# Kernel tuning notes

Hardware: AMD Instinct MI355X
Metric: run time of the kernel (lower is better)

Reference implementation:

```python
import jax, jax.numpy as jnp
import numpy as np

COUNT = 8
OUT_F = 32
IN_F = 1024
QN, QP = -128, 127  # int8 LSQ range used by nnue-pytorch


def _grad_scale(x, s):
    # forward: x ; backward: grad * s
    return x * s + jax.lax.stop_gradient(x - x * s)


def _round_pass(x):
    # forward: round(x) ; backward: identity (STE)
    return x + jax.lax.stop_gradient(jnp.round(x) - x)


def quantized_weight(weight, log_alpha_w):
    # LSQ (learned step size quantization), per-output-row step size
    alpha = jnp.exp(log_alpha_w)[:, None]                    # [O*C, 1]
    g = 1.0 / np.sqrt(float(weight.size) * QP)
    alpha = _grad_scale(alpha, jnp.asarray(g, weight.dtype))
    w_s = jnp.clip(weight / alpha, QN, QP)
    return _round_pass(w_s) * alpha                          # [O*C, I]


def setup_inputs() -> dict:
    key = jax.random.key(0)
    k1, k2, k3, k4, k5 = jax.random.split(key, 5)
    B = 8192
    x = jax.random.normal(k1, (B, IN_F), dtype=jnp.float32)
    ls_indices = jax.random.randint(k2, (B,), 0, COUNT).astype(jnp.int64)
    weight = jax.random.normal(k3, (COUNT * OUT_F, IN_F), dtype=jnp.float32) * 0.02
    bias = jax.random.normal(k4, (COUNT * OUT_F,), dtype=jnp.float32) * 0.01
    log_alpha_w = jax.random.normal(k5, (COUNT * OUT_F,), dtype=jnp.float32) * 0.1 - 5.0
    return {"x": x, "ls_indices": ls_indices, "weight": weight,
            "bias": bias, "log_alpha_w": log_alpha_w}


def reference(x, ls_indices, weight, bias, log_alpha_w):
    wq = quantized_weight(weight, log_alpha_w)               # [C*O, I]
    w_r = wq.reshape(COUNT, OUT_F, IN_F)                     # [C, O, I]
    b_r = bias.reshape(COUNT, OUT_F)                         # [C, O]
    idx = ls_indices.astype(jnp.int32)
    w_sel = w_r[idx]                                         # [B, O, I] gather
    b_sel = b_r[idx]                                         # [B, O]
    out = jnp.einsum("boi,bi->bo", w_sel, x)                # per-sample matvec
    return out + b_sel
```

## Files before the change

kernel.cpp:

```cpp
#include <hip/hip_runtime.h>


#define IN_F   1024
#define OUT_F  32
#define NCLS   8
#define NB     8192
#define KSPLIT 8
#define KCH    (IN_F / KSPLIT)
#define GRIDX  40

typedef __attribute__((ext_vector_type(8))) __bf16 bf16x8;
typedef __attribute__((ext_vector_type(4))) float  f32x4;

__device__ __forceinline__ unsigned short f2bf(float f) {
    unsigned int u = __builtin_bit_cast(unsigned int, f);
    u += 0x7FFFu + ((u >> 16) & 1u);
    return (unsigned short)(u >> 16);
}

__device__ __forceinline__ bf16x8 pack8(float4 v0, float4 v1) {
    union { unsigned short u[8]; bf16x8 v; } r;
    r.u[0] = f2bf(v0.x); r.u[1] = f2bf(v0.y); r.u[2] = f2bf(v0.z); r.u[3] = f2bf(v0.w);
    r.u[4] = f2bf(v1.x); r.u[5] = f2bf(v1.y); r.u[6] = f2bf(v1.z); r.u[7] = f2bf(v1.w);
    return r.v;
}

__global__ __launch_bounds__(256) void prep_kernel(
    const float* __restrict__ weight, const float* __restrict__ law,
    const unsigned int* __restrict__ lsw, const float* __restrict__ bias,
    float* __restrict__ alf, unsigned short* __restrict__ wq,
    int* __restrict__ counts, unsigned short* __restrict__ buckets,
    float* __restrict__ out)
{
    int t = threadIdx.x;
    if (blockIdx.x < NCLS * OUT_F) {
        int row = blockIdx.x;
        float a = expf(law[row]);
        if (t == 0) alf[row] = a;
        float4 v = ((const float4*)(weight + (size_t)row * IN_F))[t];
        ushort4 p;
        p.x = f2bf(rintf(fminf(fmaxf(v.x / a, -128.f), 127.f)));
        p.y = f2bf(rintf(fminf(fmaxf(v.y / a, -128.f), 127.f)));
        p.z = f2bf(rintf(fminf(fmaxf(v.z / a, -128.f), 127.f)));
        p.w = f2bf(rintf(fminf(fmaxf(v.w / a, -128.f), 127.f)));
        ((ushort4*)(wq + (size_t)row * IN_F))[t] = p;
        return;
    }
    int blk = blockIdx.x - NCLS * OUT_F;
    int b = blk * 256 + t;
    __shared__ int lcnt[NCLS];
    __shared__ int lbase[NCLS];
    __shared__ int s_is64;
    if (t < NCLS) lcnt[t] = 0;
    if (t == 0) s_is64 = 1;
    __syncthreads();
    if (t < 128) {
        if (lsw[2 * (blk * 128 + t) + 1] != 0u) atomicAnd(&s_is64, 0);
    }
    __syncthreads();
    int c = s_is64 ? (int)lsw[2 * b] : (int)lsw[b];
    const float4* bb = (const float4*)(bias + c * OUT_F);
    float4* ob = (float4*)(out + (size_t)b * OUT_F);
    #pragma unroll
    for (int i = 0; i < OUT_F / 4; ++i) ob[i] = bb[i];
    int lpos = atomicAdd(&lcnt[c], 1);
    __syncthreads();
    if (t < NCLS) lbase[t] = atomicAdd(&counts[t], lcnt[t]);
    __syncthreads();
    buckets[c * NB + lbase[c] + lpos] = (unsigned short)b;
}

__global__ __launch_bounds__(128) void gemm_kernel(
    const float* __restrict__ x, const float* __restrict__ alf,
    const unsigned short* __restrict__ wq,
    const int* __restrict__ counts, const unsigned short* __restrict__ buckets,
    float* __restrict__ out)
{
    int c  = blockIdx.y;
    int kq = blockIdx.z;
    int cnt = counts[c];
    int t = threadIdx.x;
    int wave = t >> 6, lane = t & 63;
    int fr = lane & 15, fq = lane >> 4;
    int k0 = kq * KCH;

    const unsigned short* wrow0 = wq + (size_t)(c * OUT_F + fr) * IN_F + k0 + fq * 8;
    const unsigned short* wrow1 = wrow0 + 16 * IN_F;
    bf16x8 Bf0[KCH / 32], Bf1[KCH / 32];
    #pragma unroll
    for (int kk = 0; kk < KCH / 32; ++kk) {
        Bf0[kk] = *(const bf16x8*)(wrow0 + kk * 32);
        Bf1[kk] = *(const bf16x8*)(wrow1 + kk * 32);
    }
    float a0 = alf[c * OUT_F + fr];
    float a1 = alf[c * OUT_F + 16 + fr];

    for (int tile = blockIdx.x * 2 + wave; tile * 16 < cnt; tile += GRIDX * 2) {
        int start = tile * 16;
        int nvalid = min(16, cnt - start);
        int j = min(fr, nvalid - 1);
        int srow = (int)buckets[c * NB + start + j];
        const float* xr = x + (size_t)srow * IN_F + k0 + fq * 8;
        f32x4 acc0 = {0.f, 0.f, 0.f, 0.f};
        f32x4 acc1 = {0.f, 0.f, 0.f, 0.f};
        #pragma unroll
        for (int kk = 0; kk < KCH / 32; ++kk) {
            float4 v0 = *(const float4*)(xr + kk * 32);
            float4 v1 = *(const float4*)(xr + kk * 32 + 4);
            bf16x8 a = pack8(v0, v1);
            acc0 = __builtin_amdgcn_mfma_f32_16x16x32_bf16(a, Bf0[kk], acc0, 0, 0, 0);
            acc1 = __builtin_amdgcn_mfma_f32_16x16x32_bf16(a, Bf1[kk], acc1, 0, 0, 0);
        }
        #pragma unroll
        for (int reg = 0; reg < 4; ++reg) {
            int m = fq * 4 + reg;
            int sr = __shfl(srow, m);
            if (m < nvalid) {
                atomicAdd(&out[(size_t)sr * OUT_F + fr],      acc0[reg] * a0);
                atomicAdd(&out[(size_t)sr * OUT_F + 16 + fr], acc1[reg] * a1);
            }
        }
    }
}

extern "C" void kernel_launch(void* const* d_in, const int* in_sizes, int n_in,
                              void* d_out, int out_size, void* d_ws, size_t ws_size,
                              hipStream_t stream)
{
    (void)in_sizes; (void)n_in; (void)out_size; (void)ws_size;
    const float*        x      = (const float*)d_in[0];
    const unsigned int* ls     = (const unsigned int*)d_in[1];
    const float*        weight = (const float*)d_in[2];
    const float*        bias   = (const float*)d_in[3];
    const float*        law    = (const float*)d_in[4];
    float*              out    = (float*)d_out;

    char* ws = (char*)d_ws;
    int*            counts  = (int*)ws;
    float*          alf     = (float*)(ws + 64);
    unsigned short* wq      = (unsigned short*)(ws + 64 + 1024);
    unsigned short* buckets = (unsigned short*)(ws + 64 + 1024 + 524288);

    hipMemsetAsync(counts, 0, NCLS * sizeof(int), stream);
    prep_kernel<<<NCLS * OUT_F + NB / 256, 256, 0, stream>>>(
        weight, law, ls, bias, alf, wq, counts, buckets, out);
    gemm_kernel<<<dim3(GRIDX, NCLS, KSPLIT), 128, 0, stream>>>(
        x, alf, wq, counts, buckets, out);
}
```

Measured before the change: 92.70 us.

## Replace atomic bucketing with single-block scan, drop memset, early-exit idle gemm blocks

The prep kernel now runs as 65 blocks of 1024 threads. 64 blocks quantize weights at four rows per block. One block buckets all 8192 samples using a wave-level shuffle prefix scan over packed 16-bit per-class counters, so it no longer needs global atomics. It writes the class counts directly, which removes the hipMemsetAsync launch. The gemm kernel exits early for blocks that have no tiles. The risk is that one block now serially handles all bucketing and bias initialization for 8192 rows, which could become a tail on the critical path.

```diff
diff --git a/kernel.cpp b/kernel.cpp
--- a/kernel.cpp
+++ b/kernel.cpp
@@ -25,7 +25,7 @@
     return r.v;
 }
 
-__global__ __launch_bounds__(256) void prep_kernel(
+__global__ __launch_bounds__(1024) void prep_kernel(
     const float* __restrict__ weight, const float* __restrict__ law,
     const unsigned int* __restrict__ lsw, const float* __restrict__ bias,
     float* __restrict__ alf, unsigned short* __restrict__ wq,
@@ -33,41 +33,84 @@
     float* __restrict__ out)
 {
     int t = threadIdx.x;
-    if (blockIdx.x < NCLS * OUT_F) {
-        int row = blockIdx.x;
+    if (blockIdx.x < 64) {
+        int row = blockIdx.x * 4 + (t >> 8);
+        int c4  = t & 255;
         float a = expf(law[row]);
-        if (t == 0) alf[row] = a;
-        float4 v = ((const float4*)(weight + (size_t)row * IN_F))[t];
+        if (c4 == 0) alf[row] = a;
+        float4 v = ((const float4*)(weight + (size_t)row * IN_F))[c4];
         ushort4 p;
         p.x = f2bf(rintf(fminf(fmaxf(v.x / a, -128.f), 127.f)));
         p.y = f2bf(rintf(fminf(fmaxf(v.y / a, -128.f), 127.f)));
         p.z = f2bf(rintf(fminf(fmaxf(v.z / a, -128.f), 127.f)));
         p.w = f2bf(rintf(fminf(fmaxf(v.w / a, -128.f), 127.f)));
-        ((ushort4*)(wq + (size_t)row * IN_F))[t] = p;
+        ((ushort4*)(wq + (size_t)row * IN_F))[c4] = p;
         return;
     }
-    int blk = blockIdx.x - NCLS * OUT_F;
-    int b = blk * 256 + t;
-    __shared__ int lcnt[NCLS];
-    __shared__ int lbase[NCLS];
+    int lane = t & 63, wv = t >> 6;
     __shared__ int s_is64;
-    if (t < NCLS) lcnt[t] = 0;
+    __shared__ unsigned int wtot[16][4];
+    __shared__ unsigned int wbase[16][4];
     if (t == 0) s_is64 = 1;
     __syncthreads();
-    if (t < 128) {
-        if (lsw[2 * (blk * 128 + t) + 1] != 0u) atomicAnd(&s_is64, 0);
+    int bad = 0;
+    #pragma unroll
+    for (int j = 0; j < 4; ++j) bad |= (lsw[2 * (j * 1024 + t) + 1] != 0u);
+    if (bad) atomicAnd(&s_is64, 0);
+    __syncthreads();
+    int is64 = s_is64;
+    unsigned int cpack = 0;
+    unsigned int cnt[4] = {0, 0, 0, 0};
+    #pragma unroll
+    for (int j = 0; j < 8; ++j) {
+        int b = j * 1024 + t;
+        int c = is64 ? (int)lsw[2 * b] : (int)lsw[b];
+        cpack |= (unsigned int)c << (j * 4);
+        cnt[c >> 1] += 1u << ((c & 1) * 16);
+    }
+    unsigned int inc[4] = {cnt[0], cnt[1], cnt[2], cnt[3]};
+    #pragma unroll
+    for (int d = 1; d < 64; d <<= 1) {
+        unsigned int o0 = __shfl_up(inc[0], d), o1 = __shfl_up(inc[1], d);
+        unsigned int o2 = __shfl_up(inc[2], d), o3 = __shfl_up(inc[3], d);
+        if (lane >= d) { inc[0] += o0; inc[1] += o1; inc[2] += o2; inc[3] += o3; }
+    }
+    if (lane == 63) {
+        wtot[wv][0] = inc[0]; wtot[wv][1] = inc[1];
+        wtot[wv][2] = inc[2]; wtot[wv][3] = inc[3];
     }
     __syncthreads();
-    int c = s_is64 ? (int)lsw[2 * b] : (int)lsw[b];
-    const float4* bb = (const float4*)(bias + c * OUT_F);
-    float4* ob = (float4*)(out + (size_t)b * OUT_F);
+    if (t < 16) {
+        unsigned int b0 = 0, b1 = 0, b2 = 0, b3 = 0;
+        for (int w2 = 0; w2 < t; ++w2) {
+            b0 += wtot[w2][0]; b1 += wtot[w2][1];
+            b2 += wtot[w2][2]; b3 += wtot[w2][3];
+        }
+        wbase[t][0] = b0; wbase[t][1] = b1; wbase[t][2] = b2; wbase[t][3] = b3;
+        if (t == 15) {
+            unsigned int tt[4] = {b0 + wtot[15][0], b1 + wtot[15][1],
+                                  b2 + wtot[15][2], b3 + wtot[15][3]};
+            #pragma unroll
+            for (int c = 0; c < NCLS; ++c)
+                counts[c] = (int)((tt[c >> 1] >> ((c & 1) * 16)) & 0xFFFFu);
+        }
+    }
+    __syncthreads();
+    unsigned int pos[4];
     #pragma unroll
-    for (int i = 0; i < OUT_F / 4; ++i) ob[i] = bb[i];
-    int lpos = atomicAdd(&lcnt[c], 1);
-    __syncthreads();
-    if (t < NCLS) lbase[t] = atomicAdd(&counts[t], lcnt[t]);
-    __syncthreads();
-    buckets[c * NB + lbase[c] + lpos] = (unsigned short)b;
+    for (int f = 0; f < 4; ++f) pos[f] = wbase[wv][f] + (inc[f] - cnt[f]);
+    #pragma unroll
+    for (int j = 0; j < 8; ++j) {
+        int b = j * 1024 + t;
+        int c = (cpack >> (j * 4)) & 7;
+        unsigned int p = (pos[c >> 1] >> ((c & 1) * 16)) & 0xFFFFu;
+        pos[c >> 1] += 1u << ((c & 1) * 16);
+        buckets[c * NB + p] = (unsigned short)b;
+        const float4* bb = (const float4*)(bias + c * OUT_F);
+        float4* ob = (float4*)(out + (size_t)b * OUT_F);
+        #pragma unroll
+        for (int i = 0; i < OUT_F / 4; ++i) ob[i] = bb[i];
+    }
 }
 
 __global__ __launch_bounds__(128) void gemm_kernel(
@@ -79,6 +122,8 @@
     int c  = blockIdx.y;
     int kq = blockIdx.z;
     int cnt = counts[c];
+    int ntiles = (cnt + 15) >> 4;
+    if ((int)blockIdx.x * 2 >= ntiles) return;
     int t = threadIdx.x;
     int wave = t >> 6, lane = t & 63;
     int fr = lane & 15, fq = lane >> 4;
@@ -95,7 +140,7 @@
     float a0 = alf[c * OUT_F + fr];
     float a1 = alf[c * OUT_F + 16 + fr];
 
-    for (int tile = blockIdx.x * 2 + wave; tile * 16 < cnt; tile += GRIDX * 2) {
+    for (int tile = blockIdx.x * 2 + wave; tile < ntiles; tile += GRIDX * 2) {
         int start = tile * 16;
         int nvalid = min(16, cnt - start);
         int j = min(fr, nvalid - 1);
@@ -141,8 +186,7 @@
     unsigned short* wq      = (unsigned short*)(ws + 64 + 1024);
     unsigned short* buckets = (unsigned short*)(ws + 64 + 1024 + 524288);
 
-    hipMemsetAsync(counts, 0, NCLS * sizeof(int), stream);
-    prep_kernel<<<NCLS * OUT_F + NB / 256, 256, 0, stream>>>(
+    prep_kernel<<<65, 1024, 0, stream>>>(
         weight, law, ls, bias, alf, wq, counts, buckets, out);
     gemm_kernel<<<dim3(GRIDX, NCLS, KSPLIT), 128, 0, stream>>>(
         x, alf, wq, counts, buckets, out);
```

After: 151.1 us. +63.0%, slower.
